# Optimization experiments

Hardware: AMD Instinct MI355X
Metric: run time of the kernel (lower is better)

The kernel has to match this reference:

```python
import jax, jax.numpy as jnp
import numpy as np

# --- static CT geometry (shapes must be static under jit; mirrors the `options` vector) ---
B = 8          # batch
V = 720        # number of projection views
D = 736        # detector bins per view
H = 512        # image height (pixels)
W = 512        # image width  (pixels)
DIMG = 0.006641            # image pixel size (physical units)
DDET = 0.0066              # detector bin size
ANG0 = 0.0                 # starting angle
DANG = 2.0 * np.pi / V     # angular step


def setup_inputs() -> dict:
    key = jax.random.key(0)
    proj = jax.random.normal(key, (B, 1, V, D), dtype=jnp.float32)
    options = jnp.array(
        [V, D, W, H, DIMG, DDET, ANG0, DANG, 5.95, 4.906, 0.0, 2.0],
        dtype=jnp.float32,
    )
    return {"proj": proj, "options": options}


def _backproject(sino):
    """Pixel-driven parallel-beam back-projection of one sinogram [V, D] -> image [H, W]."""
    xs = (jnp.arange(W, dtype=jnp.float32) - (W - 1) / 2.0) * DIMG   # pixel-center x
    ys = ((H - 1) / 2.0 - jnp.arange(H, dtype=jnp.float32)) * DIMG   # pixel-center y
    x = jnp.broadcast_to(xs[None, :], (H, W))
    y = jnp.broadcast_to(ys[:, None], (H, W))
    angles = ANG0 + jnp.arange(V, dtype=jnp.float32) * DANG

    def body(acc, inp):
        ang, row = inp                               # row: [D] detector samples at this view
        t = x * jnp.cos(ang) + y * jnp.sin(ang)      # ray coordinate of each pixel
        u = t / DDET + (D - 1) / 2.0                 # fractional detector index
        u0 = jnp.floor(u)
        w = u - u0
        i0 = u0.astype(jnp.int32)
        i1 = i0 + 1
        v0 = jnp.where((i0 >= 0) & (i0 < D), row[jnp.clip(i0, 0, D - 1)], 0.0)
        v1 = jnp.where((i1 >= 0) & (i1 < D), row[jnp.clip(i1, 0, D - 1)], 0.0)
        return acc + (1.0 - w) * v0 + w * v1, None

    acc, _ = jax.lax.scan(body, jnp.zeros((H, W), jnp.float32), (angles, sino))
    return acc * DANG  # angular integration weight


def reference(proj, options):
    # `options` carries the geometry; its shape-determining entries are baked in statically.
    sino = proj.reshape(B, V, D)
    img = jax.vmap(_backproject)(sino)
    return img.reshape(B, 1, H, W)
```

## Files before the change

kernel.cpp:

```cpp
#include <hip/hip_runtime.h>

#define BATCH 8
#define NVIEW 720
#define NPAIR 360
#define NGRP  180
#define NDET  736
#define IMGH  512
#define IMGW  512

#define DANG_F  ((float)(6.283185307179586 / 720.0))
#define RATIO_F ((float)(0.006641 / 0.0066))
#define UCENTER ((float)((NDET - 1) * 0.5))

#define PADDET 768
#define NITER  90
#define ITER_BYTES 12288
#define WS_BYTES ((size_t)BATCH * NITER * PADDET * 16)

typedef float  v2f __attribute__((ext_vector_type(2)));
typedef __fp16 v2h __attribute__((ext_vector_type(2)));
typedef __fp16 v8h __attribute__((ext_vector_type(8)));

struct alignas(16) E16 { v2h ag, bg, am, bm; };

__global__ __launch_bounds__(192) void prep_kernel(
    const float* __restrict__ proj, E16* __restrict__ ws)
{
    const int t = threadIdx.x;
    const int flat = (int)blockIdx.y * 90 + (int)blockIdx.x;
    const int b = flat & 7;
    const int p = flat >> 3;
    const int g = (p < 89) ? p + 1   : 0;
    const int m = (p < 89) ? 179 - p : 90;
    const int i = 4 * t;
    const float* __restrict__ base = proj + (size_t)b * NVIEW * NDET;
    const float* __restrict__ fA = base + (size_t)g * NDET;
    const float* __restrict__ rA = fA + (size_t)NPAIR * NDET;
    const float* __restrict__ fB = fA + (size_t)NGRP * NDET;
    const float* __restrict__ rB = fB + (size_t)NPAIR * NDET;
    const float* __restrict__ fM = base + (size_t)m * NDET;
    const float* __restrict__ rM = fM + (size_t)NPAIR * NDET;
    const float* __restrict__ fN = fM + (size_t)NGRP * NDET;
    const float* __restrict__ rN = fN + (size_t)NPAIR * NDET;

    const float4 fa = *(const float4*)(fA + i);
    const float4 ra = *(const float4*)(rA + (732 - i));
    const float4 fb = *(const float4*)(fB + i);
    const float4 rb = *(const float4*)(rB + (732 - i));
    const float4 fm = *(const float4*)(fM + i);
    const float4 rm = *(const float4*)(rM + (732 - i));
    const float4 fn = *(const float4*)(fN + i);
    const float4 rn = *(const float4*)(rN + (732 - i));

    float fa1 = __shfl_down(fa.x, 1), ra1 = __shfl_down(ra.w, 1);
    float fb1 = __shfl_down(fb.x, 1), rb1 = __shfl_down(rb.w, 1);
    float fm1 = __shfl_down(fm.x, 1), rm1 = __shfl_down(rm.w, 1);
    float fn1 = __shfl_down(fn.x, 1), rn1 = __shfl_down(rn.w, 1);
    if ((t & 63) == 63) {
        fa1 = fA[i + 4]; ra1 = rA[731 - i];
        fb1 = fB[i + 4]; rb1 = rB[731 - i];
        fm1 = fM[i + 4]; rm1 = rM[731 - i];
        fn1 = fN[i + 4]; rn1 = rN[731 - i];
    }

    if (t >= 184) return;

    const float sA[5] = {fa.x + ra.w, fa.y + ra.z, fa.z + ra.y,
                         fa.w + ra.x, fa1 + ra1};
    const float sB[5] = {fb.x + rb.w, fb.y + rb.z, fb.z + rb.y,
                         fb.w + rb.x, fb1 + rb1};
    const float sM[5] = {fm.x + rm.w, fm.y + rm.z, fm.z + rm.y,
                         fm.w + rm.x, fm1 + rm1};
    const float sN[5] = {fn.x + rn.w, fn.y + rn.z, fn.z + rn.y,
                         fn.w + rn.x, fn1 + rn1};

    E16* __restrict__ dst = ws + ((size_t)b * NITER + p) * PADDET + i;
#pragma unroll
    for (int k = 0; k < 4; ++k) {
        E16 e;
        e.ag = __builtin_amdgcn_cvt_pkrtz(sA[k + 1] - sA[k], sA[k]);
        e.bg = __builtin_amdgcn_cvt_pkrtz(sB[k + 1] - sB[k], sB[k]);
        e.am = __builtin_amdgcn_cvt_pkrtz(sM[k + 1] - sM[k], sM[k]);
        e.bm = __builtin_amdgcn_cvt_pkrtz(sN[k + 1] - sN[k], sN[k]);
        dst[k] = e;
    }
}

#define VIS(Lp, u, r0, r1, r2, r3) do {                                      \
    const float uu_ = (u);                                                   \
    const int   ii_ = (int)uu_;                                              \
    const v2h wv_ = __builtin_amdgcn_cvt_pkrtz(                              \
        __builtin_amdgcn_fractf(uu_), 1.0f);                                 \
    const v8h E_ = (Lp)[ii_];                                                \
    r0 = __builtin_amdgcn_fdot2((v2h){E_[0], E_[1]}, wv_, r0, false);        \
    r1 = __builtin_amdgcn_fdot2((v2h){E_[2], E_[3]}, wv_, r1, false);        \
    r2 = __builtin_amdgcn_fdot2((v2h){E_[4], E_[5]}, wv_, r2, false);        \
    r3 = __builtin_amdgcn_fdot2((v2h){E_[6], E_[7]}, wv_, r3, false);        \
} while (0)

#define VIS2(Lp, O, u, p0, p1, q0, q1) do {                                  \
    const float uu_ = (u);                                                   \
    const int   ii_ = (int)uu_;                                              \
    const v2h wv_ = __builtin_amdgcn_cvt_pkrtz(                              \
        __builtin_amdgcn_fractf(uu_), 1.0f);                                 \
    const v8h E_ = (Lp)[ii_];                                                \
    const v2h ha_ = {E_[(O)], E_[(O) + 1]};                                  \
    const v2h hb_ = {E_[(O) + 2], E_[(O) + 3]};                              \
    p0 = __builtin_amdgcn_fdot2(ha_, wv_, p0, false);                        \
    p1 = __builtin_amdgcn_fdot2(ha_, wv_, p1, false);                        \
    q0 = __builtin_amdgcn_fdot2(hb_, wv_, q0, false);                        \
    q1 = __builtin_amdgcn_fdot2(hb_, wv_, q1, false);                        \
} while (0)

#define VIS1(Lp, O, u, p0, q0) do {                                          \
    const float uu_ = (u);                                                   \
    const int   ii_ = (int)uu_;                                              \
    const v2h wv_ = __builtin_amdgcn_cvt_pkrtz(                              \
        __builtin_amdgcn_fractf(uu_), 1.0f);                                 \
    const v8h E_ = (Lp)[ii_];                                                \
    p0 = __builtin_amdgcn_fdot2((v2h){E_[(O)], E_[(O) + 1]}, wv_, p0, false);\
    q0 = __builtin_amdgcn_fdot2((v2h){E_[(O) + 2], E_[(O) + 3]}, wv_, q0,    \
                                false);                                      \
} while (0)

__global__ __launch_bounds__(512, 4) void backproject_dma_kernel(
    const v8h* __restrict__ ws, float* __restrict__ out)
{
    __shared__ alignas(16) v8h lds4[4][PADDET];
    __shared__ v2f cs[NGRP];

    const int tid  = threadIdx.x;
    const int wave = tid >> 6;
    const int lane = tid & 63;

    if (tid < NGRP) {
        float s, c;
        sincosf((float)tid * DANG_F, &s, &c);
        cs[tid] = (v2f){c * RATIO_F, s * RATIO_F};
    }

    const int flat = ((int)blockIdx.z * 32 + (int)blockIdx.y) * 2
                     + (int)blockIdx.x;
    const int b    = flat & 7;
    const int tile = flat >> 3;
    const int h = (tile >> 1) * 8 + wave;
    const int w = (tile & 1) * 64 + lane;

    const bool dg = (w == h);
    const bool rm = (w > h);
    const int  H  = rm ? 255 - h : h;
    const int  W  = rm ? 255 - w : w;

    const float px  = (float)W - 255.5f;
    const float py  = 255.5f - (float)H;
    const float px2 = dg ? (-0.5f - (float)W) : py;
    const float py2 = dg ? ( 0.5f + (float)H) : px;

    const char* __restrict__ wsb =
        (const char*)(ws + (size_t)b * NITER * PADDET);

    float A0 = 0.f, A1 = 0.f, A2 = 0.f, A3 = 0.f;
    float B0 = 0.f, B1 = 0.f, B2 = 0.f, B3 = 0.f;
    float X0 = 0.f, X1 = 0.f, X2 = 0.f, X3 = 0.f;
    float Y0 = 0.f, Y1 = 0.f, Y2 = 0.f, Y3 = 0.f;

    auto issue = [&](int p) {
        const char* g0 = wsb + (size_t)p * ITER_BYTES;
        char* l0 = (char*)&lds4[p & 3][0];
        __builtin_amdgcn_global_load_lds(
            (const __attribute__((address_space(1))) void*)
                (g0 + wave * 1024 + lane * 16),
            (__attribute__((address_space(3))) void*)(l0 + wave * 1024),
            16, 0, 0);
        if (wave < 4) {
            const int s = 8 + wave;
            __builtin_amdgcn_global_load_lds(
                (const __attribute__((address_space(1))) void*)
                    (g0 + s * 1024 + lane * 16),
                (__attribute__((address_space(3))) void*)(l0 + s * 1024),
                16, 0, 0);
        }
    };

    const v2f cc = {UCENTER, UCENTER};
    auto groups = [&](int p) {
        const v8h* __restrict__ L = &lds4[p & 3][0];
        const v2f t  = cs[p + 1];
        const v2f m1 = {t.x, -t.y};
        const v2f m2 = {t.y, t.x};
        const v2f gA = __builtin_elementwise_fma(
            (v2f){px, px}, m1, (v2f){py, py} * m2);
        const v2f gB = __builtin_elementwise_fma(
            (v2f){px2, px2}, m1, (v2f){py2, py2} * m2);
        const v2f upA = cc + gA, umA = cc - gA;
        const v2f upB = cc + gB, umB = cc - gB;
        VIS(L, upA.x, A0, A1, X2, X3);
        VIS(L, umA.x, A2, A3, X0, X1);
        VIS(L, upA.y, A3, A0, X3, X0);
        VIS(L, umA.y, A1, A2, X1, X2);
        VIS(L, upB.x, B2, B3, Y0, Y1);
        VIS(L, umB.x, B0, B1, Y2, Y3);
        VIS(L, upB.y, B1, B2, Y1, Y2);
        VIS(L, umB.y, B3, B0, Y3, Y0);
    };

    issue(0);
    issue(1);
    __syncthreads();

    for (int k = 0; k < 44; ++k) {
        issue(2 * k + 2);
        issue(2 * k + 3);
        groups(2 * k);
        groups(2 * k + 1);
        __syncthreads();
    }
    groups(88);

    {
        const v8h* __restrict__ L = &lds4[1][0];
        const v2f t0 = cs[0], t45 = cs[90];
        if (!dg) {
            const float g1 = px * t0.x + py * t0.y;
            const float g2 = -px * t0.y + py * t0.x;
            VIS2(L, 0, UCENTER + g1, A0, X1, A1, X2);
            VIS2(L, 0, UCENTER - g1, A2, X3, A3, X0);
            VIS2(L, 0, UCENTER + g2, A3, X2, A0, X3);
            VIS2(L, 0, UCENTER - g2, A1, X0, A2, X1);
            const float h1 = px * t45.x + py * t45.y;
            const float h2 = -px * t45.y + py * t45.x;
            VIS2(L, 4, UCENTER + h1, A0, X2, A1, X3);
            VIS2(L, 4, UCENTER - h1, A2, X0, A3, X1);
            VIS2(L, 4, UCENTER + h2, A3, X3, A0, X0);
            VIS2(L, 4, UCENTER - h2, A1, X1, A2, X2);
        } else {
            const float g1  = px * t0.x + py * t0.y;
            const float g1b = px2 * t0.x + py2 * t0.y;
            VIS2(L, 0, UCENTER + g1,  A0, A1, A1, A2);
            VIS2(L, 0, UCENTER - g1,  A2, A3, A0, A3);
            VIS2(L, 0, UCENTER + g1b, B2, B3, B3, B0);
            VIS2(L, 0, UCENTER - g1b, B0, B1, B2, B1);
            {
                const v2h wv_ = __builtin_amdgcn_cvt_pkrtz(0.5f, 1.0f);
                const v8h E_ = L[367];
                const v2h ha_ = {E_[4], E_[5]};
                const v2h hb_ = {E_[6], E_[7]};
                A0 = __builtin_amdgcn_fdot2(ha_, wv_, A0, false);
                A2 = __builtin_amdgcn_fdot2(ha_, wv_, A2, false);
                B2 = __builtin_amdgcn_fdot2(ha_, wv_, B2, false);
                B0 = __builtin_amdgcn_fdot2(ha_, wv_, B0, false);
                A1 = __builtin_amdgcn_fdot2(hb_, wv_, A1, false);
                A3 = __builtin_amdgcn_fdot2(hb_, wv_, A3, false);
                B3 = __builtin_amdgcn_fdot2(hb_, wv_, B3, false);
                B1 = __builtin_amdgcn_fdot2(hb_, wv_, B1, false);
            }
            const float e1 = (px + px) * t45.x;
            const float e2 = (px2 + px2) * t45.x;
            VIS1(L, 4, UCENTER + e1, A1, A2);
            VIS1(L, 4, UCENTER - e1, A3, A0);
            VIS1(L, 4, UCENTER + e2, B3, B0);
            VIS1(L, 4, UCENTER - e2, B1, B2);
        }
    }

    const float aE0 = dg ? X0 : Y0, aE1 = dg ? X1 : Y1;
    const float aE2 = dg ? X2 : Y2, aE3 = dg ? X3 : Y3;
    const float bE0 = dg ? Y0 : X0, bE1 = dg ? Y1 : X1;
    const float bE2 = dg ? Y2 : X2, bE3 = dg ? Y3 : X3;
    const float a0 = (A0 + aE0) * DANG_F, a1 = (A1 + aE1) * DANG_F;
    const float a2 = (A2 + aE2) * DANG_F, a3 = (A3 + aE3) * DANG_F;
    const float b0 = (B0 + bE0) * DANG_F, b1 = (B1 + bE1) * DANG_F;
    const float b2 = (B2 + bE2) * DANG_F, b3 = (B3 + bE3) * DANG_F;

    float* __restrict__ o = out + (size_t)b * IMGH * IMGW;
    const int Qr = dg ? 256 + H : W;
    const int Qc = dg ? 256 + W : H;
    o[H * IMGW + W]                         = a0;
    o[(511 - W) * IMGW + H]                 = a1;
    o[(511 - H) * IMGW + (511 - W)]         = a2;
    o[W * IMGW + (511 - H)]                 = a3;
    o[Qr * IMGW + Qc]                       = b0;
    o[(511 - Qc) * IMGW + Qr]               = b1;
    o[(511 - Qr) * IMGW + (511 - Qc)]       = b2;
    o[Qc * IMGW + (511 - Qr)]               = b3;
}

struct Stage { float4 f4, r4; float f1, r1; };

__device__ __forceinline__ void fb_load(const float* __restrict__ sino,
                                        int k, int t, Stage& S) {
    if (t < 368) {
        const int p  = (t >= 184);
        const int i  = 4 * (t - 184 * p);
        const int vf = k + 180 * p;
        const float* __restrict__ fwd = sino + vf * NDET;
        const float* __restrict__ rev = sino + (vf + NPAIR) * NDET;
        S.f4 = *(const float4*)(fwd + i);
        S.f1 = fwd[i + 4];
        S.r4 = *(const float4*)(rev + (732 - i));
        S.r1 = rev[731 - i];
    }
}

__device__ __forceinline__ void fb_write(v2h* __restrict__ L, int t,
                                         const Stage& S) {
    if (t < 368) {
        const int p = (t >= 184);
        const int i = 4 * (t - 184 * p);
        const float s0 = S.f4.x + S.r4.w;
        const float s1 = S.f4.y + S.r4.z;
        const float s2 = S.f4.z + S.r4.y;
        const float s3 = S.f4.w + S.r4.x;
        const float s4 = S.f1 + S.r1;
        const v2h n0 = __builtin_amdgcn_cvt_pkrtz(s1 - s0, s0);
        const v2h n1 = __builtin_amdgcn_cvt_pkrtz(s2 - s1, s1);
        const v2h n2 = __builtin_amdgcn_cvt_pkrtz(s3 - s2, s2);
        const v2h n3 = __builtin_amdgcn_cvt_pkrtz(s4 - s3, s3);
        struct alignas(16) H4 { v2h a, b, c, d; };
        *(H4*)(L + p * NDET + i) = H4{n0, n1, n2, n3};
    }
}

__device__ __forceinline__ void fb_visit(const v2h* __restrict__ L,
                                         float u, float& accA, float& accB) {
    const int   i0 = (int)u;
    const float fr = __builtin_amdgcn_fractf(u);
    const v2h wv = __builtin_amdgcn_cvt_pkrtz(fr, 1.0f);
    const v2h A = L[i0];
    const v2h B = L[i0 + NDET];
    accA = __builtin_amdgcn_fdot2(A, wv, accA, false);
    accB = __builtin_amdgcn_fdot2(B, wv, accB, false);
}

__global__ __launch_bounds__(512, 4) void backproject_fb_kernel(
    const float* __restrict__ proj, float* __restrict__ out)
{
    __shared__ alignas(16) v2h lds[2][2][2 * NDET];
    __shared__ v2f cs[NGRP];

    const int tid = threadIdx.x;
    if (tid < NGRP) {
        float s, c;
        sincosf((float)tid * DANG_F, &s, &c);
        cs[tid] = (v2f){c * RATIO_F, s * RATIO_F};
    }

    const int b    = blockIdx.z;
    const int lane = tid & 63;
    const int h    = (int)blockIdx.y * 8 + (tid >> 6);
    const int w0   = (int)blockIdx.x * 64 + lane;

    const float px = (float)w0 - (float)(IMGW - 1) * 0.5f;
    const float py = (float)(IMGH - 1) * 0.5f - (float)h;

    const float* __restrict__ sino = proj + (size_t)b * NVIEW * NDET;

    float a0 = 0.f, a1 = 0.f, a2 = 0.f, a3 = 0.f;
    float b0 = 0.f, b1 = 0.f, b2 = 0.f, b3 = 0.f;

    Stage s0 = {}, s1 = {};
    fb_load(sino, 0, tid, s0);
    fb_load(sino, 1, tid, s1);
    fb_write(lds[0][0], tid, s0);
    fb_write(lds[0][1], tid, s1);
    fb_load(sino, 2, tid, s0);
    fb_load(sino, 3, tid, s1);
    __syncthreads();

    for (int gg = 0; gg < NGRP; gg += 2) {
        const int buf = (gg >> 1) & 1;
#pragma unroll
        for (int sub = 0; sub < 2; ++sub) {
            const v2h* __restrict__ L = lds[buf][sub];
            const v2f t = cs[gg + sub];
            const v2f m1 = {t.x, -t.y};
            const v2f m2 = {t.y, t.x};
            const v2f pxv = {px, px};
            const v2f pyv = {py, py};
            const v2f gvec = __builtin_elementwise_fma(pxv, m1, pyv * m2);
            const v2f cc = {UCENTER, UCENTER};
            const v2f up = cc + gvec;
            const v2f um = cc - gvec;
            const v2f dd = {128.0f, 128.0f};
            const v2f dm = dd * m1;
            const v2f vp = up + dm;
            const v2f vm = um - dm;

            fb_visit(L, up.x, a0, a1);
            fb_visit(L, um.x, a2, a3);
            fb_visit(L, up.y, a3, a0);
            fb_visit(L, um.y, a1, a2);
            fb_visit(L, vp.x, b0, b1);
            fb_visit(L, vm.x, b2, b3);
            fb_visit(L, vp.y, b3, b0);
            fb_visit(L, vm.y, b1, b2);
        }
        if (gg < NGRP - 2) {
            fb_write(lds[buf ^ 1][0], tid, s0);
            fb_write(lds[buf ^ 1][1], tid, s1);
            if (gg < NGRP - 4) {
                fb_load(sino, gg + 4, tid, s0);
                fb_load(sino, gg + 5, tid, s1);
            }
            __syncthreads();
        }
    }

    float* __restrict__ o = out + (size_t)b * IMGH * IMGW;
    const int hm  = (IMGH - 1) - h;
    const int w1  = w0 + 128;
    const int wm0 = (IMGW - 1) - w0;
    const int wm1 = (IMGW - 1) - w1;
    o[h   * IMGW + w0 ] = a0 * DANG_F;
    o[wm0 * IMGW + h  ] = a1 * DANG_F;
    o[hm  * IMGW + wm0] = a2 * DANG_F;
    o[w0  * IMGW + hm ] = a3 * DANG_F;
    o[h   * IMGW + w1 ] = b0 * DANG_F;
    o[wm1 * IMGW + h  ] = b1 * DANG_F;
    o[hm  * IMGW + wm1] = b2 * DANG_F;
    o[w1  * IMGW + hm ] = b3 * DANG_F;
}

extern "C" void kernel_launch(void* const* d_in, const int* in_sizes, int n_in,
                              void* d_out, int out_size, void* d_ws, size_t ws_size,
                              hipStream_t stream) {
    const float* proj = (const float*)d_in[0];
    float* out = (float*)d_out;

    if (ws_size >= WS_BYTES) {
        E16* ws = (E16*)d_ws;
        prep_kernel<<<dim3(90, BATCH), 192, 0, stream>>>(proj, ws);
        backproject_dma_kernel<<<dim3(2, 32, BATCH), 512, 0, stream>>>(
            (const v8h*)ws, out);
    } else {
        backproject_fb_kernel<<<dim3(2, 32, BATCH), 512, 0, stream>>>(proj, out);
    }
}
```

Before: 138.7 us.

## Fuse prep and backprojection into one kernel with per-batch atomic barrier

```diff
diff --git a/kernel.cpp b/kernel.cpp
--- a/kernel.cpp
+++ b/kernel.cpp
@@ -16,6 +16,7 @@
 #define NITER  90
 #define ITER_BYTES 12288
 #define WS_BYTES ((size_t)BATCH * NITER * PADDET * 16)
+#define CTR_BYTES 1024
 
 typedef float  v2f __attribute__((ext_vector_type(2)));
 typedef __fp16 v2h __attribute__((ext_vector_type(2)));
@@ -23,65 +24,37 @@
 
 struct alignas(16) E16 { v2h ag, bg, am, bm; };
 
-__global__ __launch_bounds__(192) void prep_kernel(
-    const float* __restrict__ proj, E16* __restrict__ ws)
-{
-    const int t = threadIdx.x;
-    const int flat = (int)blockIdx.y * 90 + (int)blockIdx.x;
-    const int b = flat & 7;
-    const int p = flat >> 3;
+__device__ __forceinline__ void fuse5(const float* __restrict__ fwd,
+                                      const float* __restrict__ rev,
+                                      int i, float s[5]) {
+    const float4 f4 = *(const float4*)(fwd + i);
+    const float  f1 = fwd[i + 4];
+    const float4 r4 = *(const float4*)(rev + (732 - i));
+    const float  r1 = rev[731 - i];
+    s[0] = f4.x + r4.w; s[1] = f4.y + r4.z; s[2] = f4.z + r4.y;
+    s[3] = f4.w + r4.x; s[4] = f1 + r1;
+}
+
+__device__ __forceinline__ void prep_unit(const float* __restrict__ proj,
+                                          E16* __restrict__ ws,
+                                          int b, int p, int t) {
     const int g = (p < 89) ? p + 1   : 0;
     const int m = (p < 89) ? 179 - p : 90;
     const int i = 4 * t;
     const float* __restrict__ base = proj + (size_t)b * NVIEW * NDET;
-    const float* __restrict__ fA = base + (size_t)g * NDET;
-    const float* __restrict__ rA = fA + (size_t)NPAIR * NDET;
-    const float* __restrict__ fB = fA + (size_t)NGRP * NDET;
-    const float* __restrict__ rB = fB + (size_t)NPAIR * NDET;
-    const float* __restrict__ fM = base + (size_t)m * NDET;
-    const float* __restrict__ rM = fM + (size_t)NPAIR * NDET;
-    const float* __restrict__ fN = fM + (size_t)NGRP * NDET;
-    const float* __restrict__ rN = fN + (size_t)NPAIR * NDET;
-
-    const float4 fa = *(const float4*)(fA + i);
-    const float4 ra = *(const float4*)(rA + (732 - i));
-    const float4 fb = *(const float4*)(fB + i);
-    const float4 rb = *(const float4*)(rB + (732 - i));
-    const float4 fm = *(const float4*)(fM + i);
-    const float4 rm = *(const float4*)(rM + (732 - i));
-    const float4 fn = *(const float4*)(fN + i);
-    const float4 rn = *(const float4*)(rN + (732 - i));
-
-    float fa1 = __shfl_down(fa.x, 1), ra1 = __shfl_down(ra.w, 1);
-    float fb1 = __shfl_down(fb.x, 1), rb1 = __shfl_down(rb.w, 1);
-    float fm1 = __shfl_down(fm.x, 1), rm1 = __shfl_down(rm.w, 1);
-    float fn1 = __shfl_down(fn.x, 1), rn1 = __shfl_down(rn.w, 1);
-    if ((t & 63) == 63) {
-        fa1 = fA[i + 4]; ra1 = rA[731 - i];
-        fb1 = fB[i + 4]; rb1 = rB[731 - i];
-        fm1 = fM[i + 4]; rm1 = rM[731 - i];
-        fn1 = fN[i + 4]; rn1 = rN[731 - i];
-    }
-
-    if (t >= 184) return;
-
-    const float sA[5] = {fa.x + ra.w, fa.y + ra.z, fa.z + ra.y,
-                         fa.w + ra.x, fa1 + ra1};
-    const float sB[5] = {fb.x + rb.w, fb.y + rb.z, fb.z + rb.y,
-                         fb.w + rb.x, fb1 + rb1};
-    const float sM[5] = {fm.x + rm.w, fm.y + rm.z, fm.z + rm.y,
-                         fm.w + rm.x, fm1 + rm1};
-    const float sN[5] = {fn.x + rn.w, fn.y + rn.z, fn.z + rn.y,
-                         fn.w + rn.x, fn1 + rn1};
-
+    float sAg[5], sBg[5], sAm[5], sBm[5];
+    fuse5(base + (size_t)g * NDET,         base + (size_t)(g + 360) * NDET, i, sAg);
+    fuse5(base + (size_t)(g + 180) * NDET, base + (size_t)(g + 540) * NDET, i, sBg);
+    fuse5(base + (size_t)m * NDET,         base + (size_t)(m + 360) * NDET, i, sAm);
+    fuse5(base + (size_t)(m + 180) * NDET, base + (size_t)(m + 540) * NDET, i, sBm);
     E16* __restrict__ dst = ws + ((size_t)b * NITER + p) * PADDET + i;
 #pragma unroll
     for (int k = 0; k < 4; ++k) {
         E16 e;
-        e.ag = __builtin_amdgcn_cvt_pkrtz(sA[k + 1] - sA[k], sA[k]);
-        e.bg = __builtin_amdgcn_cvt_pkrtz(sB[k + 1] - sB[k], sB[k]);
-        e.am = __builtin_amdgcn_cvt_pkrtz(sM[k + 1] - sM[k], sM[k]);
-        e.bm = __builtin_amdgcn_cvt_pkrtz(sN[k + 1] - sN[k], sN[k]);
+        e.ag = __builtin_amdgcn_cvt_pkrtz(sAg[k + 1] - sAg[k], sAg[k]);
+        e.bg = __builtin_amdgcn_cvt_pkrtz(sBg[k + 1] - sBg[k], sBg[k]);
+        e.am = __builtin_amdgcn_cvt_pkrtz(sAm[k + 1] - sAm[k], sAm[k]);
+        e.bm = __builtin_amdgcn_cvt_pkrtz(sBm[k + 1] - sBm[k], sBm[k]);
         dst[k] = e;
     }
 }
@@ -123,12 +96,10 @@
                                 false);                                      \
 } while (0)
 
-__global__ __launch_bounds__(512, 4) void backproject_dma_kernel(
-    const v8h* __restrict__ ws, float* __restrict__ out)
+__device__ __forceinline__ void bp_compute(
+    const v8h* __restrict__ ws, float* __restrict__ out, int flat,
+    v8h (*__restrict__ lds4)[PADDET], v2f* __restrict__ cs)
 {
-    __shared__ alignas(16) v8h lds4[4][PADDET];
-    __shared__ v2f cs[NGRP];
-
     const int tid  = threadIdx.x;
     const int wave = tid >> 6;
     const int lane = tid & 63;
@@ -139,8 +110,6 @@
         cs[tid] = (v2f){c * RATIO_F, s * RATIO_F};
     }
 
-    const int flat = ((int)blockIdx.z * 32 + (int)blockIdx.y) * 2
-                     + (int)blockIdx.x;
     const int b    = flat & 7;
     const int tile = flat >> 3;
     const int h = (tile >> 1) * 8 + wave;
@@ -285,6 +254,113 @@
     o[Qc * IMGW + (511 - Qr)]               = b3;
 }
 
+__global__ __launch_bounds__(512, 4) void fused2_kernel(
+    const float* __restrict__ proj, E16* __restrict__ ws,
+    float* __restrict__ out, unsigned int* __restrict__ ctr)
+{
+    __shared__ alignas(16) v8h lds4[4][PADDET];
+    __shared__ v2f cs[NGRP];
+
+    const int tid  = threadIdx.x;
+    const int flat = ((int)blockIdx.z * 32 + (int)blockIdx.y) * 2
+                     + (int)blockIdx.x;
+    const int b    = flat & 7;
+    const int tile = flat >> 3;
+
+    if (tid < 184) {
+        prep_unit(proj, ws, b, tile, tid);
+    } else if (tid < 368 && tile < 26) {
+        prep_unit(proj, ws, b, 64 + tile, tid - 184);
+    }
+
+    __threadfence();
+    __syncthreads();
+    unsigned int* my = ctr + b * 32;
+    if (tid == 0) {
+        __hip_atomic_fetch_add(my, 1u, __ATOMIC_RELEASE,
+                               __HIP_MEMORY_SCOPE_AGENT);
+        while (__hip_atomic_load(my, __ATOMIC_ACQUIRE,
+                                 __HIP_MEMORY_SCOPE_AGENT) < 64u)
+            __builtin_amdgcn_s_sleep(16);
+    }
+    __syncthreads();
+
+    bp_compute((const v8h*)ws, out, flat, lds4, cs);
+}
+
+__global__ __launch_bounds__(192) void prep_kernel(
+    const float* __restrict__ proj, E16* __restrict__ ws)
+{
+    const int t = threadIdx.x;
+    const int flat = (int)blockIdx.y * 90 + (int)blockIdx.x;
+    const int b = flat & 7;
+    const int p = flat >> 3;
+    const int g = (p < 89) ? p + 1   : 0;
+    const int m = (p < 89) ? 179 - p : 90;
+    const int i = 4 * t;
+    const float* __restrict__ base = proj + (size_t)b * NVIEW * NDET;
+    const float* __restrict__ fA = base + (size_t)g * NDET;
+    const float* __restrict__ rA = fA + (size_t)NPAIR * NDET;
+    const float* __restrict__ fB = fA + (size_t)NGRP * NDET;
+    const float* __restrict__ rB = fB + (size_t)NPAIR * NDET;
+    const float* __restrict__ fM = base + (size_t)m * NDET;
+    const float* __restrict__ rM = fM + (size_t)NPAIR * NDET;
+    const float* __restrict__ fN = fM + (size_t)NGRP * NDET;
+    const float* __restrict__ rN = fN + (size_t)NPAIR * NDET;
+
+    const float4 fa = *(const float4*)(fA + i);
+    const float4 ra = *(const float4*)(rA + (732 - i));
+    const float4 fb = *(const float4*)(fB + i);
+    const float4 rb = *(const float4*)(rB + (732 - i));
+    const float4 fm = *(const float4*)(fM + i);
+    const float4 rm = *(const float4*)(rM + (732 - i));
+    const float4 fn = *(const float4*)(fN + i);
+    const float4 rn = *(const float4*)(rN + (732 - i));
+
+    float fa1 = __shfl_down(fa.x, 1), ra1 = __shfl_down(ra.w, 1);
+    float fb1 = __shfl_down(fb.x, 1), rb1 = __shfl_down(rb.w, 1);
+    float fm1 = __shfl_down(fm.x, 1), rm1 = __shfl_down(rm.w, 1);
+    float fn1 = __shfl_down(fn.x, 1), rn1 = __shfl_down(rn.w, 1);
+    if ((t & 63) == 63) {
+        fa1 = fA[i + 4]; ra1 = rA[731 - i];
+        fb1 = fB[i + 4]; rb1 = rB[731 - i];
+        fm1 = fM[i + 4]; rm1 = rM[731 - i];
+        fn1 = fN[i + 4]; rn1 = rN[731 - i];
+    }
+
+    if (t >= 184) return;
+
+    const float sA[5] = {fa.x + ra.w, fa.y + ra.z, fa.z + ra.y,
+                         fa.w + ra.x, fa1 + ra1};
+    const float sB[5] = {fb.x + rb.w, fb.y + rb.z, fb.z + rb.y,
+                         fb.w + rb.x, fb1 + rb1};
+    const float sM[5] = {fm.x + rm.w, fm.y + rm.z, fm.z + rm.y,
+                         fm.w + rm.x, fm1 + rm1};
+    const float sN[5] = {fn.x + rn.w, fn.y + rn.z, fn.z + rn.y,
+                         fn.w + rn.x, fn1 + rn1};
+
+    E16* __restrict__ dst = ws + ((size_t)b * NITER + p) * PADDET + i;
+#pragma unroll
+    for (int k = 0; k < 4; ++k) {
+        E16 e;
+        e.ag = __builtin_amdgcn_cvt_pkrtz(sA[k + 1] - sA[k], sA[k]);
+        e.bg = __builtin_amdgcn_cvt_pkrtz(sB[k + 1] - sB[k], sB[k]);
+        e.am = __builtin_amdgcn_cvt_pkrtz(sM[k + 1] - sM[k], sM[k]);
+        e.bm = __builtin_amdgcn_cvt_pkrtz(sN[k + 1] - sN[k], sN[k]);
+        dst[k] = e;
+    }
+}
+
+__global__ __launch_bounds__(512, 4) void backproject_dma_kernel(
+    const v8h* __restrict__ ws, float* __restrict__ out)
+{
+    __shared__ alignas(16) v8h lds4[4][PADDET];
+    __shared__ v2f cs[NGRP];
+    const int flat = ((int)blockIdx.z * 32 + (int)blockIdx.y) * 2
+                     + (int)blockIdx.x;
+    bp_compute(ws, out, flat, lds4, cs);
+}
+
 struct Stage { float4 f4, r4; float f1, r1; };
 
 __device__ __forceinline__ void fb_load(const float* __restrict__ sino,
@@ -427,7 +503,12 @@
     const float* proj = (const float*)d_in[0];
     float* out = (float*)d_out;
 
-    if (ws_size >= WS_BYTES) {
+    if (ws_size >= WS_BYTES + CTR_BYTES) {
+        E16* ws = (E16*)d_ws;
+        unsigned int* ctr = (unsigned int*)((char*)d_ws + WS_BYTES);
+        hipMemsetAsync(ctr, 0, CTR_BYTES, stream);
+        fused2_kernel<<<dim3(2, 32, BATCH), 512, 0, stream>>>(proj, ws, out, ctr);
+    } else if (ws_size >= WS_BYTES) {
         E16* ws = (E16*)d_ws;
         prep_kernel<<<dim3(90, BATCH), 192, 0, stream>>>(proj, ws);
         backproject_dma_kernel<<<dim3(2, 32, BATCH), 512, 0, stream>>>(
```

After: 295.8 us. 113% more time.
